# Kernel optimization log

Hardware: AMD Instinct MI355X
Metric: run time of the kernel (lower is better)

Reference implementation:

```python
import jax, jax.numpy as jnp
import numpy as np

N = 500000      # num nodes
D = 128         # node feature dim == out_features
HOPS = 3        # num_samples hops


def setup_inputs() -> dict:
    key = jax.random.key(0)
    k1, k2, k3 = jax.random.split(key, 3)
    feature = jax.random.normal(k1, (N, D), dtype=jnp.float32)
    # Linear(in_features=2*D, out_features=D): W is [in, out] layout here
    W = jax.random.normal(k2, (2 * D, D), dtype=jnp.float32) / np.sqrt(2.0 * D)
    b = jnp.zeros((D,), dtype=jnp.float32)
    neigh_idx = jax.random.randint(k3, (HOPS, N), 0, N, dtype=jnp.int64)
    return {"feature": feature, "W": W, "b": b, "neigh_idx": neigh_idx}


def reference(feature, W, b, neigh_idx):
    # Per hop: gather sampled neighbor features, concat with running state,
    # dense linear projection. ReLU applied once at the end (as in source).
    out = feature  # [N, D]
    for i in range(HOPS):
        neighbor_features = feature[neigh_idx[i]]          # irregular gather [N, D]
        cat = jnp.concatenate((out, neighbor_features), axis=1)  # [N, 2D]
        out = cat @ W + b                                   # [N, D]
    return jax.nn.relu(out)
```

## Files before the change

### kernel.cpp

```cpp
#include <hip/hip_runtime.h>
#include <hip/hip_bf16.h>

#define NNODES 500000
#define DFEAT  128

typedef __attribute__((ext_vector_type(8))) short    bf16x8;
typedef __attribute__((ext_vector_type(4))) float    f32x4;
typedef __attribute__((ext_vector_type(4))) float    float4v;
typedef __attribute__((ext_vector_type(8))) unsigned short ushort8;

static __device__ __forceinline__ unsigned short f2bf(float f) {
    unsigned u = __builtin_bit_cast(unsigned, f);
    unsigned r = u + 0x7FFF + ((u >> 16) & 1);
    return (unsigned short)(r >> 16);
}

__global__ void cvt_bf16_kernel(const float* __restrict__ in,
                                unsigned short* __restrict__ out, int nchunk8) {
    int i = blockIdx.x * blockDim.x + threadIdx.x;
    int stride = gridDim.x * blockDim.x;
    for (; i < nchunk8; i += stride) {
        float4v a = ((const float4v*)in)[2 * i];
        float4v b = ((const float4v*)in)[2 * i + 1];
        ushort8 o;
        o[0] = f2bf(a.x); o[1] = f2bf(a.y); o[2] = f2bf(a.z); o[3] = f2bf(a.w);
        o[4] = f2bf(b.x); o[5] = f2bf(b.y); o[6] = f2bf(b.z); o[7] = f2bf(b.w);
        ((ushort8*)out)[i] = o;
    }
}

__global__ void pack_w_kernel(const float* __restrict__ W,
                              unsigned short* __restrict__ Wp) {
    int c = blockIdx.x * blockDim.x + threadIdx.x;
    if (c >= 4096) return;
    int l  = c & 63;
    int t  = c >> 6;
    int kk = t >> 3, n = t & 7;
    ushort8 o;
    #pragma unroll
    for (int i = 0; i < 8; ++i) {
        int k   = kk * 32 + (l >> 4) * 8 + i;
        int col = n * 16 + (l & 15);
        o[i] = f2bf(W[k * 128 + col]);
    }
    ((ushort8*)Wp)[c] = o;
}

template<int FINAL>
__global__ __launch_bounds__(512, 4) void hop_kernel(
    const unsigned short* __restrict__ state,
    const unsigned short* __restrict__ feat,
    const int*            __restrict__ idx,
    const unsigned short* __restrict__ Wp,
    const float*          __restrict__ bias,
    unsigned short*       __restrict__ out_b,
    float*                __restrict__ out_f)
{
    __shared__ __align__(16) unsigned short Wl[32768];
    int t = threadIdx.x;
    for (int j = t; j < 4096; j += 512)
        ((ushort8*)Wl)[j] = ((const ushort8*)Wp)[j];
    __syncthreads();

    int wave = t >> 6, lane = t & 63;
    int rowtile = blockIdx.x * 256 + wave * 32;
    int ar  = lane & 15;
    int sub = (lane >> 4) * 8;

    int r0 = rowtile + ar, r1 = r0 + 16;
    int cr0 = min(r0, NNODES - 1), cr1 = min(r1, NNODES - 1);
    int g0 = idx[cr0], g1 = idx[cr1];

    const unsigned short* s0 = state + (size_t)cr0 * 128 + sub;
    const unsigned short* s1 = state + (size_t)cr1 * 128 + sub;
    const unsigned short* f0 = feat  + (size_t)g0  * 128 + sub;
    const unsigned short* f1 = feat  + (size_t)g1  * 128 + sub;

    f32x4 acc[2][8];
    #pragma unroll
    for (int r = 0; r < 2; ++r)
        #pragma unroll
        for (int n = 0; n < 8; ++n)
            acc[r][n] = f32x4{0.f, 0.f, 0.f, 0.f};

    #pragma unroll
    for (int kk = 0; kk < 8; ++kk) {
        const unsigned short* p0 = (kk < 4) ? s0 + kk * 32 : f0 + (kk - 4) * 32;
        const unsigned short* p1 = (kk < 4) ? s1 + kk * 32 : f1 + (kk - 4) * 32;
        bf16x8 a0 = *(const bf16x8*)p0;
        bf16x8 a1 = *(const bf16x8*)p1;
        #pragma unroll
        for (int n = 0; n < 8; ++n) {
            bf16x8 b = *(const bf16x8*)&Wl[(size_t)((kk * 8 + n) * 64 + lane) * 8];
            acc[0][n] = __builtin_amdgcn_mfma_f32_16x16x32_bf16(a0, b, acc[0][n], 0, 0, 0);
            acc[1][n] = __builtin_amdgcn_mfma_f32_16x16x32_bf16(a1, b, acc[1][n], 0, 0, 0);
        }
    }

    int crow = (lane >> 4) * 4;
    int ccol = lane & 15;
    #pragma unroll
    for (int n = 0; n < 8; ++n) {
        float bv = bias[n * 16 + ccol];
        #pragma unroll
        for (int r = 0; r < 2; ++r) {
            int rb = rowtile + r * 16 + crow;
            #pragma unroll
            for (int i = 0; i < 4; ++i) {
                int row = rb + i;
                if (row < NNODES) {
                    float v = acc[r][n][i] + bv;
                    size_t off = (size_t)row * 128 + n * 16 + ccol;
                    if (FINAL) out_f[off] = fmaxf(v, 0.f);
                    else       out_b[off] = f2bf(v);
                }
            }
        }
    }
}

extern "C" void kernel_launch(void* const* d_in, const int* in_sizes, int n_in,
                              void* d_out, int out_size, void* d_ws, size_t ws_size,
                              hipStream_t stream) {
    const float* feature = (const float*)d_in[0];
    const float* W       = (const float*)d_in[1];
    const float* bias    = (const float*)d_in[2];
    const int*   idx     = (const int*)d_in[3];

    unsigned short* Wp        = (unsigned short*)d_ws;
    unsigned short* feature_b = (unsigned short*)((char*)d_ws + 65536);
    unsigned short* s2        = (unsigned short*)((char*)d_ws + 65536 + (size_t)NNODES * 128 * 2);
    unsigned short* s1        = (unsigned short*)d_out;
    float*          outf      = (float*)d_out;

    const int nchunk8 = NNODES * DFEAT / 8;
    cvt_bf16_kernel<<<2048, 256, 0, stream>>>(feature, feature_b, nchunk8);
    pack_w_kernel<<<16, 256, 0, stream>>>(W, Wp);

    const int grid = (NNODES + 255) / 256;
    hop_kernel<0><<<grid, 512, 0, stream>>>(feature_b, feature_b, idx,              Wp, bias, s1, nullptr);
    hop_kernel<0><<<grid, 512, 0, stream>>>(s1,        feature_b, idx + NNODES,     Wp, bias, s2, nullptr);
    hop_kernel<1><<<grid, 512, 0, stream>>>(s2,        feature_b, idx + 2 * NNODES, Wp, bias, nullptr, outf);
}
```

Measured before the change: 758.7 us.

## Permute weight columns for vectorized stores and prefetch A rows before LDS sync

Packed W columns are permuted so each lane owns 8 contiguous output columns. The epilogue can then write 16-byte vectors (ushort8 or two float4) instead of scattered scalar stores. Each wave now handles 16 rows instead of 32, so the grid doubles and per-block W loads into LDS double too. All A-operand global loads (state and gathered neighbour rows) are issued before the barrier so they overlap the W staging into LDS, at the cost of more register pressure and more redundant W loading.

```diff
diff --git a/kernel.cpp b/kernel.cpp
--- a/kernel.cpp
+++ b/kernel.cpp
@@ -40,7 +40,7 @@
     #pragma unroll
     for (int i = 0; i < 8; ++i) {
         int k   = kk * 32 + (l >> 4) * 8 + i;
-        int col = n * 16 + (l & 15);
+        int col = (l & 15) * 8 + n;
         o[i] = f2bf(W[k * 128 + col]);
     }
     ((ushort8*)Wp)[c] = o;
@@ -58,62 +58,64 @@
 {
     __shared__ __align__(16) unsigned short Wl[32768];
     int t = threadIdx.x;
-    for (int j = t; j < 4096; j += 512)
-        ((ushort8*)Wl)[j] = ((const ushort8*)Wp)[j];
-    __syncthreads();
-
     int wave = t >> 6, lane = t & 63;
-    int rowtile = blockIdx.x * 256 + wave * 32;
+    int rowtile = blockIdx.x * 128 + wave * 16;
     int ar  = lane & 15;
     int sub = (lane >> 4) * 8;
 
-    int r0 = rowtile + ar, r1 = r0 + 16;
-    int cr0 = min(r0, NNODES - 1), cr1 = min(r1, NNODES - 1);
-    int g0 = idx[cr0], g1 = idx[cr1];
+    int r0  = rowtile + ar;
+    int cr0 = min(r0, NNODES - 1);
+    int gi  = idx[cr0];
+
+    for (int j = t; j < 4096; j += 512)
+        ((ushort8*)Wl)[j] = ((const ushort8*)Wp)[j];
 
     const unsigned short* s0 = state + (size_t)cr0 * 128 + sub;
-    const unsigned short* s1 = state + (size_t)cr1 * 128 + sub;
-    const unsigned short* f0 = feat  + (size_t)g0  * 128 + sub;
-    const unsigned short* f1 = feat  + (size_t)g1  * 128 + sub;
+    const unsigned short* f0 = feat  + (size_t)gi  * 128 + sub;
+    bf16x8 A[8];
+    #pragma unroll
+    for (int kk = 0; kk < 4; ++kk) A[kk]     = *(const bf16x8*)(s0 + kk * 32);
+    #pragma unroll
+    for (int kk = 0; kk < 4; ++kk) A[4 + kk] = *(const bf16x8*)(f0 + kk * 32);
 
-    f32x4 acc[2][8];
+    __syncthreads();
+
+    f32x4 acc[8];
     #pragma unroll
-    for (int r = 0; r < 2; ++r)
-        #pragma unroll
-        for (int n = 0; n < 8; ++n)
-            acc[r][n] = f32x4{0.f, 0.f, 0.f, 0.f};
+    for (int n = 0; n < 8; ++n) acc[n] = f32x4{0.f, 0.f, 0.f, 0.f};
 
     #pragma unroll
     for (int kk = 0; kk < 8; ++kk) {
-        const unsigned short* p0 = (kk < 4) ? s0 + kk * 32 : f0 + (kk - 4) * 32;
-        const unsigned short* p1 = (kk < 4) ? s1 + kk * 32 : f1 + (kk - 4) * 32;
-        bf16x8 a0 = *(const bf16x8*)p0;
-        bf16x8 a1 = *(const bf16x8*)p1;
         #pragma unroll
         for (int n = 0; n < 8; ++n) {
             bf16x8 b = *(const bf16x8*)&Wl[(size_t)((kk * 8 + n) * 64 + lane) * 8];
-            acc[0][n] = __builtin_amdgcn_mfma_f32_16x16x32_bf16(a0, b, acc[0][n], 0, 0, 0);
-            acc[1][n] = __builtin_amdgcn_mfma_f32_16x16x32_bf16(a1, b, acc[1][n], 0, 0, 0);
+            acc[n] = __builtin_amdgcn_mfma_f32_16x16x32_bf16(A[kk], b, acc[n], 0, 0, 0);
         }
     }
 
     int crow = (lane >> 4) * 4;
     int ccol = lane & 15;
+    float4v b0 = *(const float4v*)&bias[ccol * 8];
+    float4v b1 = *(const float4v*)&bias[ccol * 8 + 4];
     #pragma unroll
-    for (int n = 0; n < 8; ++n) {
-        float bv = bias[n * 16 + ccol];
-        #pragma unroll
-        for (int r = 0; r < 2; ++r) {
-            int rb = rowtile + r * 16 + crow;
-            #pragma unroll
-            for (int i = 0; i < 4; ++i) {
-                int row = rb + i;
-                if (row < NNODES) {
-                    float v = acc[r][n][i] + bv;
-                    size_t off = (size_t)row * 128 + n * 16 + ccol;
-                    if (FINAL) out_f[off] = fmaxf(v, 0.f);
-                    else       out_b[off] = f2bf(v);
-                }
+    for (int i = 0; i < 4; ++i) {
+        int row = rowtile + crow + i;
+        if (row < NNODES) {
+            float v0 = acc[0][i] + b0.x, v1 = acc[1][i] + b0.y;
+            float v2 = acc[2][i] + b0.z, v3 = acc[3][i] + b0.w;
+            float v4 = acc[4][i] + b1.x, v5 = acc[5][i] + b1.y;
+            float v6 = acc[6][i] + b1.z, v7 = acc[7][i] + b1.w;
+            size_t off = (size_t)row * 128 + ccol * 8;
+            if (FINAL) {
+                float4v o0 = {fmaxf(v0, 0.f), fmaxf(v1, 0.f), fmaxf(v2, 0.f), fmaxf(v3, 0.f)};
+                float4v o1 = {fmaxf(v4, 0.f), fmaxf(v5, 0.f), fmaxf(v6, 0.f), fmaxf(v7, 0.f)};
+                *(float4v*)&out_f[off]     = o0;
+                *(float4v*)&out_f[off + 4] = o1;
+            } else {
+                ushort8 o;
+                o[0] = f2bf(v0); o[1] = f2bf(v1); o[2] = f2bf(v2); o[3] = f2bf(v3);
+                o[4] = f2bf(v4); o[5] = f2bf(v5); o[6] = f2bf(v6); o[7] = f2bf(v7);
+                *(ushort8*)&out_b[off] = o;
             }
         }
     }
@@ -137,7 +139,7 @@
     cvt_bf16_kernel<<<2048, 256, 0, stream>>>(feature, feature_b, nchunk8);
     pack_w_kernel<<<16, 256, 0, stream>>>(W, Wp);
 
-    const int grid = (NNODES + 255) / 256;
+    const int grid = (NNODES + 127) / 128;
     hop_kernel<0><<<grid, 512, 0, stream>>>(feature_b, feature_b, idx,              Wp, bias, s1, nullptr);
     hop_kernel<0><<<grid, 512, 0, stream>>>(s1,        feature_b, idx + NNODES,     Wp, bias, s2, nullptr);
     hop_kernel<1><<<grid, 512, 0, stream>>>(s2,        feature_b, idx + 2 * NNODES, Wp, bias, nullptr, outf);
```

New measurement: 668.3 us. 1.14x faster.
